# Optimization experiments

Hardware: AMD Instinct MI355X
Metric: run time of the kernel (lower is better)

The kernel has to match this reference:

```python
import jax, jax.numpy as jnp
import numpy as np
from jax import lax

SCORE_THRESHOLD = 0.001
IOU_THRESHOLD = 0.7
MAX_DETECTIONS = 300
PRE_NMS_TOPK = 1024      # standard pre-NMS candidate cap (torchvision/YOLO practice)
CLASS_OFFSET = 4096.0    # > max image coord, separates classes so cross-class IoU == 0
IMG = 640.0

B, N, C = 32, 8400, 80


def setup_inputs() -> dict:
    key = jax.random.key(0)
    kc, ks, kp = jax.random.split(key, 3)
    # well-formed boxes in [y1, x1, y2, x2] convention (matches repo's nms())
    tl = jax.random.uniform(kc, (B, N, 2), jnp.float32, 0.0, IMG - 1.0)   # (y1, x1)
    wh = jax.random.uniform(ks, (B, N, 2), jnp.float32, 4.0, 160.0)      # (h, w)
    boxes = jnp.concatenate([tl, jnp.minimum(tl + wh, IMG)], axis=-1)     # [B,N,4]
    scores = jax.random.uniform(kp, (B, N, C), jnp.float32)               # [B,N,C]
    return {"boxes": boxes, "scores": scores}


def _pairwise_iou(b):
    # b: [B,K,4] as [y1,x1,y2,x2]; +1 pixel convention per the repo's nms()
    y1, x1, y2, x2 = b[..., 0], b[..., 1], b[..., 2], b[..., 3]
    areas = (x2 - x1 + 1.0) * (y2 - y1 + 1.0)                             # [B,K]
    yy1 = jnp.maximum(y1[:, :, None], y1[:, None, :])
    xx1 = jnp.maximum(x1[:, :, None], x1[:, None, :])
    yy2 = jnp.minimum(y2[:, :, None], y2[:, None, :])
    xx2 = jnp.minimum(x2[:, :, None], x2[:, None, :])
    w = jnp.maximum(0.0, xx2 - xx1 + 1.0)
    h = jnp.maximum(0.0, yy2 - yy1 + 1.0)
    inter = w * h                                                          # [B,K,K]
    return inter / (areas[:, :, None] + areas[:, None, :] - inter)


def multiclass_nms(boxes, scores):
    b, n, c = scores.shape
    flat = jnp.where(scores > SCORE_THRESHOLD, scores, 0.0).reshape(b, n * c)
    top_scores, top_idx = lax.top_k(flat, PRE_NMS_TOPK)                    # [B,K]
    box_idx = top_idx // c
    cls_idx = top_idx % c                                                  # int32 [B,K]
    cand = jnp.take_along_axis(boxes, box_idx[..., None], axis=1)          # [B,K,4]
    # offset boxes by class so per-class NMS happens in one shared pass
    off = cand + (cls_idx.astype(cand.dtype) * CLASS_OFFSET)[..., None]
    iou = _pairwise_iou(off)                                               # [B,K,K]

    k = PRE_NMS_TOPK
    idx = jnp.arange(k)
    keep0 = top_scores > SCORE_THRESHOLD                                   # [B,K]

    def body(i, keep):
        row = iou[:, i, :]                                                 # [B,K]
        sup = (row > IOU_THRESHOLD) & keep[:, i][:, None] & (idx[None, :] > i)
        return keep & ~sup

    keep = lax.fori_loop(0, k, body, keep0)                                # greedy NMS

    final_scores = jnp.where(keep, top_scores, 0.0)
    out_scores, sel = lax.top_k(final_scores, MAX_DETECTIONS)              # [B,300]
    out_boxes = jnp.take_along_axis(cand, sel[..., None], axis=1)          # [B,300,4]
    out_labels = jnp.take_along_axis(cls_idx, sel, axis=1)                 # [B,300]
    n_valid = jnp.minimum(jnp.sum(keep, axis=1, keepdims=True), MAX_DETECTIONS)
    return out_boxes, out_scores, out_labels.astype(jnp.int32), n_valid.astype(jnp.int32)


def reference(boxes, scores):
    return multiclass_nms(boxes, scores)
```

## Files before the change

kernel.cpp:

```cpp
#include <hip/hip_runtime.h>
#include <cstdint>
#include <cstddef>

#define B_      32
#define N_      8400
#define C_      80
#define NC      672000
#define NCV4    168000
#define NBINS   4096
#define TOPK    1024
#define MAXDET  300
#define CANDCAP 4096
#define NSLICE  16
#define SLICE_V4 10500
#define STAGE_CAP 1024
#define CC_STRIDE 32

#define STAGE_THRESH 0.998046875f

#define WS_CANDCNT   0
#define WS_CANDKEYS  4096
#define WS_TOPSCORE  1052672
#define WS_TOPBOX    1183744
#define WS_TOPCLS    1708032
#define WS_KEEP      1839104
#define WS_TOTAL     1970176

#define OUT_SCORES  38400
#define OUT_LABELS  48000
#define OUT_NVALID  57600

__global__ __launch_bounds__(256) void stage_kernel(const float4* __restrict__ scores4,
                                                    unsigned* __restrict__ candCount,
                                                    unsigned long long* __restrict__ candKeys) {
    __shared__ unsigned long long stage[STAGE_CAP];
    __shared__ unsigned lcnt;
    __shared__ unsigned sbase;
    int b = blockIdx.x;
    int sl = blockIdx.y;
    int tid = threadIdx.x;
    if (tid == 0) lcnt = 0;
    __syncthreads();
    const float4* s = scores4 + (size_t)b * NCV4 + (size_t)sl * SLICE_V4;
    unsigned long long* ck = candKeys + (size_t)b * CANDCAP;
    unsigned* cc = &candCount[b * CC_STRIDE];
    for (int i = tid; i < SLICE_V4; i += 256) {
        float4 v = s[i];
        float c[4] = {v.x, v.y, v.z, v.w};
        unsigned flat0 = ((unsigned)sl * SLICE_V4 + (unsigned)i) * 4u;
        #pragma unroll
        for (int kc = 0; kc < 4; ++kc) {
            float x = (c[kc] > 0.001f) ? c[kc] : 0.0f;
            if (x >= STAGE_THRESH) {
                unsigned long long key =
                    ((unsigned long long)__float_as_uint(x) << 32) |
                    (unsigned long long)(0xFFFFFFFFu - (flat0 + kc));
                unsigned p = atomicAdd(&lcnt, 1u);
                if (p < (unsigned)STAGE_CAP) stage[p] = key;
                else {
                    unsigned gp = atomicAdd(cc, 1u);
                    if (gp < (unsigned)CANDCAP) ck[gp] = key;
                }
            }
        }
    }
    __syncthreads();
    unsigned n = lcnt < (unsigned)STAGE_CAP ? lcnt : (unsigned)STAGE_CAP;
    if (tid == 0) sbase = atomicAdd(cc, n);
    __syncthreads();
    unsigned basep = sbase;
    for (unsigned i = tid; i < n; i += 256) {
        unsigned gp = basep + i;
        if (gp < (unsigned)CANDCAP) ck[gp] = stage[i];
    }
}

__global__ __launch_bounds__(1024) void sort_gather_kernel(
        const float4* __restrict__ scores4,
        const unsigned long long* __restrict__ candKeys,
        const unsigned* __restrict__ candCount,
        const float* __restrict__ boxes,
        float* __restrict__ topScore,
        float* __restrict__ topBox,
        int* __restrict__ topCls) {
    __shared__ unsigned long long k[CANDCAP];
    __shared__ unsigned fhist[NBINS];
    __shared__ unsigned scnt;
    __shared__ int s_cut;
    int b = blockIdx.x;
    int tid = threadIdx.x;
    unsigned M = candCount[b * CC_STRIDE];
    bool fb = (M < (unsigned)TOPK) || (M > (unsigned)CANDCAP);
    int S;
    if (!fb) {
        S = (M <= 1024u) ? 1024 : (M <= 2048u ? 2048 : CANDCAP);
        const unsigned long long* ck = candKeys + (size_t)b * CANDCAP;
        for (int i = tid; i < S; i += 1024)
            k[i] = (i < (int)M) ? ck[i] : 0ull;
        __syncthreads();
    } else {
        for (int i = tid; i < NBINS; i += 1024) fhist[i] = 0;
        if (tid == 0) scnt = 0;
        __syncthreads();
        const float4* s = scores4 + (size_t)b * NCV4;
        for (int i = tid; i < NCV4; i += 1024) {
            float4 v = s[i];
            float c[4] = {v.x, v.y, v.z, v.w};
            #pragma unroll
            for (int kc = 0; kc < 4; ++kc) {
                float x = (c[kc] > 0.001f) ? c[kc] : 0.0f;
                int bin = (int)(x * 4096.0f);
                bin = bin > (NBINS - 1) ? (NBINS - 1) : bin;
                atomicAdd(&fhist[bin], 1u);
            }
        }
        __syncthreads();
        if (tid == 0) {
            unsigned acc = 0;
            int cb = 0;
            for (int bin = NBINS - 1; bin >= 0; --bin) {
                acc += fhist[bin];
                if (acc >= (unsigned)TOPK) { cb = bin; break; }
            }
            s_cut = cb;
        }
        __syncthreads();
        int cb = s_cut;
        for (int i = tid; i < NCV4; i += 1024) {
            float4 v = s[i];
            float c[4] = {v.x, v.y, v.z, v.w};
            unsigned flat0 = (unsigned)i * 4u;
            #pragma unroll
            for (int kc = 0; kc < 4; ++kc) {
                float x = (c[kc] > 0.001f) ? c[kc] : 0.0f;
                int bin = (int)(x * 4096.0f);
                bin = bin > (NBINS - 1) ? (NBINS - 1) : bin;
                if (bin >= cb) {
                    unsigned p = atomicAdd(&scnt, 1u);
                    if (p < (unsigned)CANDCAP)
                        k[p] = ((unsigned long long)__float_as_uint(x) << 32) |
                               (unsigned long long)(0xFFFFFFFFu - (flat0 + kc));
                }
            }
        }
        __syncthreads();
        unsigned M2 = scnt < (unsigned)CANDCAP ? scnt : (unsigned)CANDCAP;
        S = (M2 <= 1024u) ? 1024 : (M2 <= 2048u ? 2048 : CANDCAP);
        for (int i = tid; i < S; i += 1024)
            if (i >= (int)M2) k[i] = 0ull;
        __syncthreads();
    }
    for (int kk = 2; kk <= S; kk <<= 1) {
        for (int j = kk >> 1; j > 0; j >>= 1) {
            for (int t = tid; t < S; t += 1024) {
                int l = t ^ j;
                if (l > t) {
                    unsigned long long a = k[t], c = k[l];
                    bool sw = ((t & kk) == 0) ? (a < c) : (a > c);
                    if (sw) { k[t] = c; k[l] = a; }
                }
            }
            __syncthreads();
        }
    }
    int i = tid;
    unsigned long long key = k[i];
    float sc = __uint_as_float((unsigned)(key >> 32));
    unsigned idx = 0xFFFFFFFFu - (unsigned)(key & 0xFFFFFFFFull);
    if (idx >= (unsigned)NC) idx = 0;
    unsigned bi = idx / (unsigned)C_;
    unsigned cl = idx % (unsigned)C_;
    const float* bp = boxes + (size_t)b * N_ * 4 + (size_t)bi * 4;
    float c0 = bp[0], c1 = bp[1], c2 = bp[2], c3 = bp[3];
    topScore[b * TOPK + i] = sc;
    float* tb = topBox + ((size_t)b * TOPK + i) * 4;
    tb[0] = c0; tb[1] = c1; tb[2] = c2; tb[3] = c3;
    topCls[b * TOPK + i] = (int)cl;
}

#define CLS_CAP 256
__global__ __launch_bounds__(64) void nms_kernel(const float* __restrict__ topScore,
                                                 const float* __restrict__ topBox,
                                                 const int* __restrict__ topCls,
                                                 int* __restrict__ keep) {
    __shared__ unsigned short pos[CLS_CAP];
    __shared__ float by1[CLS_CAP], bx1[CLS_CAP], by2[CLS_CAP], bx2[CLS_CAP];
    __shared__ float barea[CLS_CAP];
    __shared__ unsigned char sup[CLS_CAP];
    int b = blockIdx.x;
    int c = blockIdx.y;
    int lane = threadIdx.x;
    const float* ts = topScore + b * TOPK;
    const int*   tc = topCls + b * TOPK;
    int*         kp = keep + b * TOPK;
    float off = (float)c * 4096.0f;
    int base = 0;
    for (int chunkS = 0; chunkS < TOPK; chunkS += 64) {
        int i = chunkS + lane;
        int cls = tc[i];
        float sc = ts[i];
        bool mine = (cls == c);
        bool listed = mine && (sc > 0.001f);
        if (mine) kp[i] = 0;
        unsigned long long mask = __ballot(listed);
        int rank = __popcll(mask & ((1ull << lane) - 1ull));
        if (listed) {
            int slot = base + rank;
            if (slot < CLS_CAP) {
                pos[slot] = (unsigned short)i;
                const float* tb = topBox + ((size_t)(b * TOPK + i)) * 4;
                float y1 = tb[0] + off, x1 = tb[1] + off;
                float y2 = tb[2] + off, x2 = tb[3] + off;
                by1[slot] = y1; bx1[slot] = x1; by2[slot] = y2; bx2[slot] = x2;
                barea[slot] = __fmul_rn((x2 - x1) + 1.0f, (y2 - y1) + 1.0f);
                sup[slot] = 0;
            }
        }
        base += __popcll(mask);
    }
    int m = base < CLS_CAP ? base : CLS_CAP;
    __syncthreads();
    int cur = 0;
    while (cur < m) {
        if (lane == 0) kp[pos[cur]] = 1;
        float cy1 = by1[cur], cx1 = bx1[cur], cy2 = by2[cur], cx2 = bx2[cur];
        float carea = barea[cur];
        for (int j = cur + 1 + lane; j < m; j += 64) {
            if (!sup[j]) {
                float yy1 = fmaxf(cy1, by1[j]), xx1 = fmaxf(cx1, bx1[j]);
                float yy2 = fminf(cy2, by2[j]), xx2 = fminf(cx2, bx2[j]);
                float w = fmaxf(0.0f, (xx2 - xx1) + 1.0f);
                float h = fmaxf(0.0f, (yy2 - yy1) + 1.0f);
                float inter = __fmul_rn(w, h);
                float denom = (carea + barea[j]) - inter;
                float iou = inter / denom;
                if (iou > 0.7f) sup[j] = 1;
            }
        }
        __syncthreads();
        int nxt = m;
        for (int j = cur + 1 + lane; j < m; j += 64)
            if (!sup[j]) { nxt = j; break; }
        for (int o = 32; o > 0; o >>= 1) {
            int other = __shfl_xor(nxt, o, 64);
            nxt = nxt < other ? nxt : other;
        }
        cur = nxt;
    }
}

__global__ __launch_bounds__(1024) void finalize_kernel(const float* __restrict__ topScore,
                                                        const float* __restrict__ topBox,
                                                        const int* __restrict__ topCls,
                                                        const int* __restrict__ keep,
                                                        float* __restrict__ out) {
    __shared__ int sk[TOPK];
    __shared__ int sel[MAXDET];
    int b = blockIdx.x;
    int i = threadIdx.x;
    int kp = keep[b * TOPK + i];
    sk[i] = kp;
    __syncthreads();
    for (int off = 1; off < TOPK; off <<= 1) {
        int add = (i >= off) ? sk[i - off] : 0;
        __syncthreads();
        sk[i] += add;
        __syncthreads();
    }
    int nk = sk[TOPK - 1];
    int incl = sk[i];
    int kexcl = incl - kp;
    int sexcl = i - kexcl;
    if (kp) {
        if (kexcl < MAXDET) sel[kexcl] = i;
    } else {
        int slot = nk + sexcl;
        if (slot < MAXDET) sel[slot] = i;
    }
    __syncthreads();
    if (i < MAXDET) {
        int p = sel[i];
        float sc = (i < nk) ? topScore[b * TOPK + p] : 0.0f;
        const float* tb = topBox + ((size_t)b * TOPK + p) * 4;
        float* ob = out + ((size_t)b * MAXDET + i) * 4;
        ob[0] = tb[0]; ob[1] = tb[1]; ob[2] = tb[2]; ob[3] = tb[3];
        out[OUT_SCORES + b * MAXDET + i] = sc;
        out[OUT_LABELS + b * MAXDET + i] = (float)topCls[b * TOPK + p];
    }
    if (i == 0) out[OUT_NVALID + b] = (float)(nk < MAXDET ? nk : MAXDET);
}

extern "C" void kernel_launch(void* const* d_in, const int* in_sizes, int n_in,
                              void* d_out, int out_size, void* d_ws, size_t ws_size,
                              hipStream_t stream) {
    const float* boxes  = (const float*)d_in[0];
    const float* scores = (const float*)d_in[1];
    float* out = (float*)d_out;
    char* ws = (char*)d_ws;

    unsigned* candCount = (unsigned*)(ws + WS_CANDCNT);
    unsigned long long* candKeys = (unsigned long long*)(ws + WS_CANDKEYS);
    float* topScore = (float*)(ws + WS_TOPSCORE);
    float* topBox = (float*)(ws + WS_TOPBOX);
    int* topCls = (int*)(ws + WS_TOPCLS);
    int* keep = (int*)(ws + WS_KEEP);

    const float4* scores4 = (const float4*)scores;

    hipMemsetAsync(candCount, 0, B_ * CC_STRIDE * sizeof(unsigned), stream);

    stage_kernel<<<dim3(B_, NSLICE), 256, 0, stream>>>(scores4, candCount, candKeys);
    sort_gather_kernel<<<B_, 1024, 0, stream>>>(scores4, candKeys, candCount, boxes,
                                                topScore, topBox, topCls);
    nms_kernel<<<dim3(B_, C_), 64, 0, stream>>>(topScore, topBox, topCls, keep);
    finalize_kernel<<<B_, 1024, 0, stream>>>(topScore, topBox, topCls, keep, out);
}
```

Baseline: 202.3 us.

## Fuse sort, NMS and finalize into one per-batch kernel with per-slice segments

```diff
diff --git a/kernel.cpp b/kernel.cpp
--- a/kernel.cpp
+++ b/kernel.cpp
@@ -13,37 +13,26 @@
 #define CANDCAP 4096
 #define NSLICE  16
 #define SLICE_V4 10500
-#define STAGE_CAP 1024
-#define CC_STRIDE 32
+#define SEGCAP  256
 
 #define STAGE_THRESH 0.998046875f
 
-#define WS_CANDCNT   0
-#define WS_CANDKEYS  4096
-#define WS_TOPSCORE  1052672
-#define WS_TOPBOX    1183744
-#define WS_TOPCLS    1708032
-#define WS_KEEP      1839104
-#define WS_TOTAL     1970176
+#define WS_CANDKEYS  0
+#define WS_SEGCNT    1048576
 
 #define OUT_SCORES  38400
 #define OUT_LABELS  48000
 #define OUT_NVALID  57600
 
 __global__ __launch_bounds__(256) void stage_kernel(const float4* __restrict__ scores4,
-                                                    unsigned* __restrict__ candCount,
+                                                    unsigned* __restrict__ segCnt,
                                                     unsigned long long* __restrict__ candKeys) {
-    __shared__ unsigned long long stage[STAGE_CAP];
     __shared__ unsigned lcnt;
-    __shared__ unsigned sbase;
-    int b = blockIdx.x;
-    int sl = blockIdx.y;
-    int tid = threadIdx.x;
+    int b = blockIdx.x, sl = blockIdx.y, tid = threadIdx.x;
     if (tid == 0) lcnt = 0;
     __syncthreads();
     const float4* s = scores4 + (size_t)b * NCV4 + (size_t)sl * SLICE_V4;
-    unsigned long long* ck = candKeys + (size_t)b * CANDCAP;
-    unsigned* cc = &candCount[b * CC_STRIDE];
+    unsigned long long* seg = candKeys + (size_t)b * CANDCAP + (size_t)sl * SEGCAP;
     for (int i = tid; i < SLICE_V4; i += 256) {
         float4 v = s[i];
         float c[4] = {v.x, v.y, v.z, v.w};
@@ -52,242 +41,257 @@
         for (int kc = 0; kc < 4; ++kc) {
             float x = (c[kc] > 0.001f) ? c[kc] : 0.0f;
             if (x >= STAGE_THRESH) {
-                unsigned long long key =
-                    ((unsigned long long)__float_as_uint(x) << 32) |
-                    (unsigned long long)(0xFFFFFFFFu - (flat0 + kc));
                 unsigned p = atomicAdd(&lcnt, 1u);
-                if (p < (unsigned)STAGE_CAP) stage[p] = key;
-                else {
-                    unsigned gp = atomicAdd(cc, 1u);
-                    if (gp < (unsigned)CANDCAP) ck[gp] = key;
-                }
-            }
-        }
-    }
-    __syncthreads();
-    unsigned n = lcnt < (unsigned)STAGE_CAP ? lcnt : (unsigned)STAGE_CAP;
-    if (tid == 0) sbase = atomicAdd(cc, n);
-    __syncthreads();
-    unsigned basep = sbase;
-    for (unsigned i = tid; i < n; i += 256) {
-        unsigned gp = basep + i;
-        if (gp < (unsigned)CANDCAP) ck[gp] = stage[i];
-    }
+                if (p < (unsigned)SEGCAP)
+                    seg[p] = ((unsigned long long)__float_as_uint(x) << 32) |
+                             (unsigned long long)(0xFFFFFFFFu - (flat0 + kc));
+            }
+        }
+    }
+    __syncthreads();
+    if (tid == 0) segCnt[b * NSLICE + sl] = lcnt;
 }
 
-__global__ __launch_bounds__(1024) void sort_gather_kernel(
+struct PhaseA {
+    unsigned long long k[CANDCAP];
+    unsigned fhist[NBINS];
+    unsigned scnt;
+    int cut;
+};
+struct PhaseB {
+    float sc[TOPK];
+    float oy1[TOPK], ox1[TOPK], oy2[TOPK], ox2[TOPK];
+    float area[TOPK];
+    float4 ob[TOPK];
+    unsigned short cls[TOPK];
+    int keep[TOPK];
+    unsigned short wps[16][TOPK];
+    int sel[MAXDET];
+};
+
+__global__ __launch_bounds__(1024) void mega_kernel(
         const float4* __restrict__ scores4,
         const unsigned long long* __restrict__ candKeys,
-        const unsigned* __restrict__ candCount,
-        const float* __restrict__ boxes,
-        float* __restrict__ topScore,
-        float* __restrict__ topBox,
-        int* __restrict__ topCls) {
-    __shared__ unsigned long long k[CANDCAP];
-    __shared__ unsigned fhist[NBINS];
-    __shared__ unsigned scnt;
-    __shared__ int s_cut;
+        const unsigned* __restrict__ segCnt,
+        const float4* __restrict__ boxes4,
+        float* __restrict__ out) {
+    __shared__ union { PhaseA a; PhaseB bb; } u;
+    __shared__ unsigned pref[NSLICE + 1];
+    __shared__ int s_fb;
     int b = blockIdx.x;
     int tid = threadIdx.x;
-    unsigned M = candCount[b * CC_STRIDE];
-    bool fb = (M < (unsigned)TOPK) || (M > (unsigned)CANDCAP);
-    int S;
-    if (!fb) {
-        S = (M <= 1024u) ? 1024 : (M <= 2048u ? 2048 : CANDCAP);
-        const unsigned long long* ck = candKeys + (size_t)b * CANDCAP;
-        for (int i = tid; i < S; i += 1024)
-            k[i] = (i < (int)M) ? ck[i] : 0ull;
-        __syncthreads();
+
+    if (tid < NSLICE) pref[tid + 1] = segCnt[b * NSLICE + tid];
+    __syncthreads();
+    if (tid == 0) {
+        unsigned acc = 0; int fb2 = 0;
+        pref[0] = 0;
+        for (int s2 = 1; s2 <= NSLICE; ++s2) {
+            unsigned c2 = pref[s2];
+            if (c2 > (unsigned)SEGCAP) fb2 = 1;
+            acc += c2;
+            pref[s2] = acc;
+        }
+        if (acc < (unsigned)TOPK || acc > (unsigned)CANDCAP) fb2 = 1;
+        s_fb = fb2;
+    }
+    __syncthreads();
+
+    unsigned M;
+    if (!s_fb) {
+        for (int s2 = 0; s2 < NSLICE; ++s2) {
+            unsigned base2 = pref[s2], n2 = pref[s2 + 1] - base2;
+            const unsigned long long* src =
+                candKeys + (size_t)b * CANDCAP + (size_t)s2 * SEGCAP;
+            for (unsigned t = tid; t < n2; t += 1024) u.a.k[base2 + t] = src[t];
+        }
+        M = pref[NSLICE];
     } else {
-        for (int i = tid; i < NBINS; i += 1024) fhist[i] = 0;
-        if (tid == 0) scnt = 0;
+        for (int i2 = tid; i2 < NBINS; i2 += 1024) u.a.fhist[i2] = 0;
+        if (tid == 0) u.a.scnt = 0;
         __syncthreads();
         const float4* s = scores4 + (size_t)b * NCV4;
-        for (int i = tid; i < NCV4; i += 1024) {
-            float4 v = s[i];
-            float c[4] = {v.x, v.y, v.z, v.w};
+        for (int i2 = tid; i2 < NCV4; i2 += 1024) {
+            float4 v = s[i2];
+            float c4[4] = {v.x, v.y, v.z, v.w};
             #pragma unroll
             for (int kc = 0; kc < 4; ++kc) {
-                float x = (c[kc] > 0.001f) ? c[kc] : 0.0f;
+                float x = (c4[kc] > 0.001f) ? c4[kc] : 0.0f;
                 int bin = (int)(x * 4096.0f);
                 bin = bin > (NBINS - 1) ? (NBINS - 1) : bin;
-                atomicAdd(&fhist[bin], 1u);
+                atomicAdd(&u.a.fhist[bin], 1u);
             }
         }
         __syncthreads();
         if (tid == 0) {
-            unsigned acc = 0;
-            int cb = 0;
+            unsigned acc = 0; int cb = 0;
             for (int bin = NBINS - 1; bin >= 0; --bin) {
-                acc += fhist[bin];
+                acc += u.a.fhist[bin];
                 if (acc >= (unsigned)TOPK) { cb = bin; break; }
             }
-            s_cut = cb;
-        }
-        __syncthreads();
-        int cb = s_cut;
-        for (int i = tid; i < NCV4; i += 1024) {
-            float4 v = s[i];
-            float c[4] = {v.x, v.y, v.z, v.w};
-            unsigned flat0 = (unsigned)i * 4u;
+            u.a.cut = cb;
+        }
+        __syncthreads();
+        int cb = u.a.cut;
+        for (int i2 = tid; i2 < NCV4; i2 += 1024) {
+            float4 v = s[i2];
+            float c4[4] = {v.x, v.y, v.z, v.w};
+            unsigned flat0 = (unsigned)i2 * 4u;
             #pragma unroll
             for (int kc = 0; kc < 4; ++kc) {
-                float x = (c[kc] > 0.001f) ? c[kc] : 0.0f;
+                float x = (c4[kc] > 0.001f) ? c4[kc] : 0.0f;
                 int bin = (int)(x * 4096.0f);
                 bin = bin > (NBINS - 1) ? (NBINS - 1) : bin;
                 if (bin >= cb) {
-                    unsigned p = atomicAdd(&scnt, 1u);
+                    unsigned p = atomicAdd(&u.a.scnt, 1u);
                     if (p < (unsigned)CANDCAP)
-                        k[p] = ((unsigned long long)__float_as_uint(x) << 32) |
-                               (unsigned long long)(0xFFFFFFFFu - (flat0 + kc));
-                }
-            }
-        }
-        __syncthreads();
-        unsigned M2 = scnt < (unsigned)CANDCAP ? scnt : (unsigned)CANDCAP;
-        S = (M2 <= 1024u) ? 1024 : (M2 <= 2048u ? 2048 : CANDCAP);
-        for (int i = tid; i < S; i += 1024)
-            if (i >= (int)M2) k[i] = 0ull;
-        __syncthreads();
-    }
-    for (int kk = 2; kk <= S; kk <<= 1) {
-        for (int j = kk >> 1; j > 0; j >>= 1) {
-            for (int t = tid; t < S; t += 1024) {
-                int l = t ^ j;
-                if (l > t) {
-                    unsigned long long a = k[t], c = k[l];
-                    bool sw = ((t & kk) == 0) ? (a < c) : (a > c);
-                    if (sw) { k[t] = c; k[l] = a; }
-                }
-            }
+                        u.a.k[p] = ((unsigned long long)__float_as_uint(x) << 32) |
+                                   (unsigned long long)(0xFFFFFFFFu - (flat0 + kc));
+                }
+            }
+        }
+        __syncthreads();
+        M = u.a.scnt;
+        if (M > (unsigned)CANDCAP) M = CANDCAP;
+    }
+    int S = (M <= 1024u) ? 1024 : (M <= 2048u ? 2048 : CANDCAP);
+    for (int i2 = tid; i2 < S; i2 += 1024)
+        if (i2 >= (int)M) u.a.k[i2] = 0ull;
+    __syncthreads();
+
+    {
+        bool crossed = false;
+        for (int kk = 2; kk <= S; kk <<= 1) {
+            int j = kk >> 1;
+            for (; j >= 128; j >>= 1) {
+                __syncthreads();
+                for (int t = tid; t < S; t += 1024) {
+                    int l = t ^ j;
+                    if (l > t) {
+                        unsigned long long a0 = u.a.k[t], c0 = u.a.k[l];
+                        bool sw = ((t & kk) == 0) ? (a0 < c0) : (a0 > c0);
+                        if (sw) { u.a.k[t] = c0; u.a.k[l] = a0; }
+                    }
+                }
+                crossed = true;
+            }
+            if (crossed) { __syncthreads(); crossed = false; }
+            int half = S >> 1;
+            for (; j >= 1; j >>= 1) {
+                for (int c2 = tid; c2 < half; c2 += 1024) {
+                    int t = ((c2 & ~(j - 1)) << 1) | (c2 & (j - 1));
+                    int l = t | j;
+                    unsigned long long a0 = u.a.k[t], c0 = u.a.k[l];
+                    bool sw = ((t & kk) == 0) ? (a0 < c0) : (a0 > c0);
+                    if (sw) { u.a.k[t] = c0; u.a.k[l] = a0; }
+                }
+                __threadfence_block();
+            }
+        }
+    }
+    __syncthreads();
+
+    unsigned long long key = u.a.k[tid];
+    __syncthreads();
+    {
+        float sc = __uint_as_float((unsigned)(key >> 32));
+        unsigned idx = 0xFFFFFFFFu - (unsigned)(key & 0xFFFFFFFFull);
+        if (idx >= (unsigned)NC) idx = 0;
+        unsigned bi = idx / (unsigned)C_;
+        unsigned cl = idx - bi * (unsigned)C_;
+        float4 bx = boxes4[(size_t)b * N_ + bi];
+        float off = (float)cl * 4096.0f;
+        float oy1 = bx.x + off, ox1 = bx.y + off;
+        float oy2 = bx.z + off, ox2 = bx.w + off;
+        u.bb.sc[tid] = sc;
+        u.bb.oy1[tid] = oy1; u.bb.ox1[tid] = ox1;
+        u.bb.oy2[tid] = oy2; u.bb.ox2[tid] = ox2;
+        u.bb.area[tid] = __fmul_rn((ox2 - ox1) + 1.0f, (oy2 - oy1) + 1.0f);
+        u.bb.ob[tid] = bx;
+        u.bb.cls[tid] = (unsigned short)cl;
+        u.bb.keep[tid] = 0;
+    }
+    __syncthreads();
+
+    {
+        int w = tid >> 6, lane = tid & 63;
+        unsigned long long lmask = (1ull << lane) - 1ull;
+        unsigned short* wp = u.bb.wps[w];
+        for (int cc = w * 5; cc < w * 5 + 5; ++cc) {
+            int nm = 0;
+            for (int chunk = 0; chunk < TOPK; chunk += 64) {
+                int i2 = chunk + lane;
+                bool listed = (u.bb.cls[i2] == (unsigned short)cc) &&
+                              (u.bb.sc[i2] > 0.001f);
+                unsigned long long mask = __ballot(listed);
+                if (listed) wp[nm + __popcll(mask & lmask)] = (unsigned short)i2;
+                nm += __popcll(mask);
+            }
+            __threadfence_block();
+            int cur = 0;
+            while (cur < nm) {
+                int pcur = wp[cur] & 0x3FF;
+                if (lane == 0) u.bb.keep[pcur] = 1;
+                float cy1 = u.bb.oy1[pcur], cx1 = u.bb.ox1[pcur];
+                float cy2 = u.bb.oy2[pcur], cx2 = u.bb.ox2[pcur];
+                float carea = u.bb.area[pcur];
+                for (int t2 = cur + 1 + lane; t2 < nm; t2 += 64) {
+                    unsigned short e = wp[t2];
+                    if (!(e & 0x8000)) {
+                        int pj = e;
+                        float yy1 = fmaxf(cy1, u.bb.oy1[pj]);
+                        float xx1 = fmaxf(cx1, u.bb.ox1[pj]);
+                        float yy2 = fminf(cy2, u.bb.oy2[pj]);
+                        float xx2 = fminf(cx2, u.bb.ox2[pj]);
+                        float w2 = fmaxf(0.0f, (xx2 - xx1) + 1.0f);
+                        float h2 = fmaxf(0.0f, (yy2 - yy1) + 1.0f);
+                        float inter = __fmul_rn(w2, h2);
+                        float denom = (carea + u.bb.area[pj]) - inter;
+                        if (inter / denom > 0.7f) wp[t2] = e | 0x8000;
+                    }
+                }
+                __threadfence_block();
+                int nxt = nm;
+                for (int t2 = cur + 1 + lane; t2 < nm; t2 += 64)
+                    if (!(wp[t2] & 0x8000)) { nxt = t2; break; }
+                for (int o = 32; o > 0; o >>= 1) {
+                    int other = __shfl_xor(nxt, o, 64);
+                    nxt = nxt < other ? nxt : other;
+                }
+                cur = nxt;
+            }
+        }
+    }
+    __syncthreads();
+
+    {
+        int kp = u.bb.keep[tid];
+        for (int off2 = 1; off2 < TOPK; off2 <<= 1) {
+            int add = (tid >= off2) ? u.bb.keep[tid - off2] : 0;
             __syncthreads();
-        }
-    }
-    int i = tid;
-    unsigned long long key = k[i];
-    float sc = __uint_as_float((unsigned)(key >> 32));
-    unsigned idx = 0xFFFFFFFFu - (unsigned)(key & 0xFFFFFFFFull);
-    if (idx >= (unsigned)NC) idx = 0;
-    unsigned bi = idx / (unsigned)C_;
-    unsigned cl = idx % (unsigned)C_;
-    const float* bp = boxes + (size_t)b * N_ * 4 + (size_t)bi * 4;
-    float c0 = bp[0], c1 = bp[1], c2 = bp[2], c3 = bp[3];
-    topScore[b * TOPK + i] = sc;
-    float* tb = topBox + ((size_t)b * TOPK + i) * 4;
-    tb[0] = c0; tb[1] = c1; tb[2] = c2; tb[3] = c3;
-    topCls[b * TOPK + i] = (int)cl;
-}
-
-#define CLS_CAP 256
-__global__ __launch_bounds__(64) void nms_kernel(const float* __restrict__ topScore,
-                                                 const float* __restrict__ topBox,
-                                                 const int* __restrict__ topCls,
-                                                 int* __restrict__ keep) {
-    __shared__ unsigned short pos[CLS_CAP];
-    __shared__ float by1[CLS_CAP], bx1[CLS_CAP], by2[CLS_CAP], bx2[CLS_CAP];
-    __shared__ float barea[CLS_CAP];
-    __shared__ unsigned char sup[CLS_CAP];
-    int b = blockIdx.x;
-    int c = blockIdx.y;
-    int lane = threadIdx.x;
-    const float* ts = topScore + b * TOPK;
-    const int*   tc = topCls + b * TOPK;
-    int*         kp = keep + b * TOPK;
-    float off = (float)c * 4096.0f;
-    int base = 0;
-    for (int chunkS = 0; chunkS < TOPK; chunkS += 64) {
-        int i = chunkS + lane;
-        int cls = tc[i];
-        float sc = ts[i];
-        bool mine = (cls == c);
-        bool listed = mine && (sc > 0.001f);
-        if (mine) kp[i] = 0;
-        unsigned long long mask = __ballot(listed);
-        int rank = __popcll(mask & ((1ull << lane) - 1ull));
-        if (listed) {
-            int slot = base + rank;
-            if (slot < CLS_CAP) {
-                pos[slot] = (unsigned short)i;
-                const float* tb = topBox + ((size_t)(b * TOPK + i)) * 4;
-                float y1 = tb[0] + off, x1 = tb[1] + off;
-                float y2 = tb[2] + off, x2 = tb[3] + off;
-                by1[slot] = y1; bx1[slot] = x1; by2[slot] = y2; bx2[slot] = x2;
-                barea[slot] = __fmul_rn((x2 - x1) + 1.0f, (y2 - y1) + 1.0f);
-                sup[slot] = 0;
-            }
-        }
-        base += __popcll(mask);
-    }
-    int m = base < CLS_CAP ? base : CLS_CAP;
-    __syncthreads();
-    int cur = 0;
-    while (cur < m) {
-        if (lane == 0) kp[pos[cur]] = 1;
-        float cy1 = by1[cur], cx1 = bx1[cur], cy2 = by2[cur], cx2 = bx2[cur];
-        float carea = barea[cur];
-        for (int j = cur + 1 + lane; j < m; j += 64) {
-            if (!sup[j]) {
-                float yy1 = fmaxf(cy1, by1[j]), xx1 = fmaxf(cx1, bx1[j]);
-                float yy2 = fminf(cy2, by2[j]), xx2 = fminf(cx2, bx2[j]);
-                float w = fmaxf(0.0f, (xx2 - xx1) + 1.0f);
-                float h = fmaxf(0.0f, (yy2 - yy1) + 1.0f);
-                float inter = __fmul_rn(w, h);
-                float denom = (carea + barea[j]) - inter;
-                float iou = inter / denom;
-                if (iou > 0.7f) sup[j] = 1;
-            }
-        }
-        __syncthreads();
-        int nxt = m;
-        for (int j = cur + 1 + lane; j < m; j += 64)
-            if (!sup[j]) { nxt = j; break; }
-        for (int o = 32; o > 0; o >>= 1) {
-            int other = __shfl_xor(nxt, o, 64);
-            nxt = nxt < other ? nxt : other;
-        }
-        cur = nxt;
-    }
-}
-
-__global__ __launch_bounds__(1024) void finalize_kernel(const float* __restrict__ topScore,
-                                                        const float* __restrict__ topBox,
-                                                        const int* __restrict__ topCls,
-                                                        const int* __restrict__ keep,
-                                                        float* __restrict__ out) {
-    __shared__ int sk[TOPK];
-    __shared__ int sel[MAXDET];
-    int b = blockIdx.x;
-    int i = threadIdx.x;
-    int kp = keep[b * TOPK + i];
-    sk[i] = kp;
-    __syncthreads();
-    for (int off = 1; off < TOPK; off <<= 1) {
-        int add = (i >= off) ? sk[i - off] : 0;
-        __syncthreads();
-        sk[i] += add;
-        __syncthreads();
-    }
-    int nk = sk[TOPK - 1];
-    int incl = sk[i];
-    int kexcl = incl - kp;
-    int sexcl = i - kexcl;
-    if (kp) {
-        if (kexcl < MAXDET) sel[kexcl] = i;
-    } else {
-        int slot = nk + sexcl;
-        if (slot < MAXDET) sel[slot] = i;
-    }
-    __syncthreads();
-    if (i < MAXDET) {
-        int p = sel[i];
-        float sc = (i < nk) ? topScore[b * TOPK + p] : 0.0f;
-        const float* tb = topBox + ((size_t)b * TOPK + p) * 4;
-        float* ob = out + ((size_t)b * MAXDET + i) * 4;
-        ob[0] = tb[0]; ob[1] = tb[1]; ob[2] = tb[2]; ob[3] = tb[3];
-        out[OUT_SCORES + b * MAXDET + i] = sc;
-        out[OUT_LABELS + b * MAXDET + i] = (float)topCls[b * TOPK + p];
-    }
-    if (i == 0) out[OUT_NVALID + b] = (float)(nk < MAXDET ? nk : MAXDET);
+            u.bb.keep[tid] += add;
+            __syncthreads();
+        }
+        int nk = u.bb.keep[TOPK - 1];
+        int incl = u.bb.keep[tid];
+        int kexcl = incl - kp;
+        int sexcl = tid - kexcl;
+        if (kp) {
+            if (kexcl < MAXDET) u.bb.sel[kexcl] = tid;
+        } else {
+            int slot = nk + sexcl;
+            if (slot < MAXDET) u.bb.sel[slot] = tid;
+        }
+        __syncthreads();
+        if (tid < MAXDET) {
+            int p = u.bb.sel[tid];
+            float sc2 = (tid < nk) ? u.bb.sc[p] : 0.0f;
+            ((float4*)out)[b * MAXDET + tid] = u.bb.ob[p];
+            out[OUT_SCORES + b * MAXDET + tid] = sc2;
+            out[OUT_LABELS + b * MAXDET + tid] = (float)u.bb.cls[p];
+        }
+        if (tid == 0) out[OUT_NVALID + b] = (float)(nk < MAXDET ? nk : MAXDET);
+    }
 }
 
 extern "C" void kernel_launch(void* const* d_in, const int* in_sizes, int n_in,
@@ -298,20 +302,12 @@
     float* out = (float*)d_out;
     char* ws = (char*)d_ws;
 
-    unsigned* candCount = (unsigned*)(ws + WS_CANDCNT);
     unsigned long long* candKeys = (unsigned long long*)(ws + WS_CANDKEYS);
-    float* topScore = (float*)(ws + WS_TOPSCORE);
-    float* topBox = (float*)(ws + WS_TOPBOX);
-    int* topCls = (int*)(ws + WS_TOPCLS);
-    int* keep = (int*)(ws + WS_KEEP);
+    unsigned* segCnt = (unsigned*)(ws + WS_SEGCNT);
 
     const float4* scores4 = (const float4*)scores;
-
-    hipMemsetAsync(candCount, 0, B_ * CC_STRIDE * sizeof(unsigned), stream);
-
-    stage_kernel<<<dim3(B_, NSLICE), 256, 0, stream>>>(scores4, candCount, candKeys);
-    sort_gather_kernel<<<B_, 1024, 0, stream>>>(scores4, candKeys, candCount, boxes,
-                                                topScore, topBox, topCls);
-    nms_kernel<<<dim3(B_, C_), 64, 0, stream>>>(topScore, topBox, topCls, keep);
-    finalize_kernel<<<B_, 1024, 0, stream>>>(topScore, topBox, topCls, keep, out);
+    const float4* boxes4  = (const float4*)boxes;
+
+    stage_kernel<<<dim3(B_, NSLICE), 256, 0, stream>>>(scores4, segCnt, candKeys);
+    mega_kernel<<<B_, 1024, 0, stream>>>(scores4, candKeys, segCnt, boxes4, out);
 }
```

Result: slower. 223.2 us (+10.3%).

## Use per-slice candidate segments, drop memset, and elide intra-wave sort barriers

Applied to the files above, without the earlier changes.

```diff
diff --git a/kernel.cpp b/kernel.cpp
--- a/kernel.cpp
+++ b/kernel.cpp
@@ -13,37 +13,30 @@
 #define CANDCAP 4096
 #define NSLICE  16
 #define SLICE_V4 10500
-#define STAGE_CAP 1024
-#define CC_STRIDE 32
+#define SEGCAP  256
 
 #define STAGE_THRESH 0.998046875f
 
-#define WS_CANDCNT   0
-#define WS_CANDKEYS  4096
-#define WS_TOPSCORE  1052672
-#define WS_TOPBOX    1183744
-#define WS_TOPCLS    1708032
-#define WS_KEEP      1839104
-#define WS_TOTAL     1970176
+#define WS_CANDKEYS  0
+#define WS_SEGCNT    1048576
+#define WS_TOPSCORE  1050624
+#define WS_TOPBOX    1181696
+#define WS_TOPCLS    1705984
+#define WS_KEEP      1837056
 
 #define OUT_SCORES  38400
 #define OUT_LABELS  48000
 #define OUT_NVALID  57600
 
 __global__ __launch_bounds__(256) void stage_kernel(const float4* __restrict__ scores4,
-                                                    unsigned* __restrict__ candCount,
+                                                    unsigned* __restrict__ segCnt,
                                                     unsigned long long* __restrict__ candKeys) {
-    __shared__ unsigned long long stage[STAGE_CAP];
     __shared__ unsigned lcnt;
-    __shared__ unsigned sbase;
-    int b = blockIdx.x;
-    int sl = blockIdx.y;
-    int tid = threadIdx.x;
+    int b = blockIdx.x, sl = blockIdx.y, tid = threadIdx.x;
     if (tid == 0) lcnt = 0;
     __syncthreads();
     const float4* s = scores4 + (size_t)b * NCV4 + (size_t)sl * SLICE_V4;
-    unsigned long long* ck = candKeys + (size_t)b * CANDCAP;
-    unsigned* cc = &candCount[b * CC_STRIDE];
+    unsigned long long* seg = candKeys + (size_t)b * CANDCAP + (size_t)sl * SEGCAP;
     for (int i = tid; i < SLICE_V4; i += 256) {
         float4 v = s[i];
         float c[4] = {v.x, v.y, v.z, v.w};
@@ -52,124 +45,136 @@
         for (int kc = 0; kc < 4; ++kc) {
             float x = (c[kc] > 0.001f) ? c[kc] : 0.0f;
             if (x >= STAGE_THRESH) {
-                unsigned long long key =
-                    ((unsigned long long)__float_as_uint(x) << 32) |
-                    (unsigned long long)(0xFFFFFFFFu - (flat0 + kc));
                 unsigned p = atomicAdd(&lcnt, 1u);
-                if (p < (unsigned)STAGE_CAP) stage[p] = key;
-                else {
-                    unsigned gp = atomicAdd(cc, 1u);
-                    if (gp < (unsigned)CANDCAP) ck[gp] = key;
-                }
-            }
-        }
-    }
-    __syncthreads();
-    unsigned n = lcnt < (unsigned)STAGE_CAP ? lcnt : (unsigned)STAGE_CAP;
-    if (tid == 0) sbase = atomicAdd(cc, n);
-    __syncthreads();
-    unsigned basep = sbase;
-    for (unsigned i = tid; i < n; i += 256) {
-        unsigned gp = basep + i;
-        if (gp < (unsigned)CANDCAP) ck[gp] = stage[i];
-    }
+                if (p < (unsigned)SEGCAP)
+                    seg[p] = ((unsigned long long)__float_as_uint(x) << 32) |
+                             (unsigned long long)(0xFFFFFFFFu - (flat0 + kc));
+            }
+        }
+    }
+    __syncthreads();
+    if (tid == 0) segCnt[b * NSLICE + sl] = lcnt;
 }
 
 __global__ __launch_bounds__(1024) void sort_gather_kernel(
         const float4* __restrict__ scores4,
         const unsigned long long* __restrict__ candKeys,
-        const unsigned* __restrict__ candCount,
+        const unsigned* __restrict__ segCnt,
         const float* __restrict__ boxes,
         float* __restrict__ topScore,
         float* __restrict__ topBox,
         int* __restrict__ topCls) {
-    __shared__ unsigned long long k[CANDCAP];
-    __shared__ unsigned fhist[NBINS];
+    __shared__ union {
+        unsigned long long k[CANDCAP];
+        unsigned fh[2 * CANDCAP];
+    } u;
+    __shared__ unsigned pref[NSLICE + 1];
+    __shared__ int s_fb;
     __shared__ unsigned scnt;
     __shared__ int s_cut;
     int b = blockIdx.x;
     int tid = threadIdx.x;
-    unsigned M = candCount[b * CC_STRIDE];
-    bool fb = (M < (unsigned)TOPK) || (M > (unsigned)CANDCAP);
-    int S;
-    if (!fb) {
-        S = (M <= 1024u) ? 1024 : (M <= 2048u ? 2048 : CANDCAP);
-        const unsigned long long* ck = candKeys + (size_t)b * CANDCAP;
-        for (int i = tid; i < S; i += 1024)
-            k[i] = (i < (int)M) ? ck[i] : 0ull;
-        __syncthreads();
+
+    if (tid < NSLICE) pref[tid + 1] = segCnt[b * NSLICE + tid];
+    __syncthreads();
+    if (tid == 0) {
+        unsigned acc = 0; int fb2 = 0;
+        pref[0] = 0;
+        for (int s2 = 1; s2 <= NSLICE; ++s2) {
+            unsigned c2 = pref[s2];
+            if (c2 > (unsigned)SEGCAP) fb2 = 1;
+            acc += c2;
+            pref[s2] = acc;
+        }
+        if (acc < (unsigned)TOPK || acc > (unsigned)CANDCAP) fb2 = 1;
+        s_fb = fb2;
+    }
+    __syncthreads();
+
+    unsigned M;
+    if (!s_fb) {
+        int w = tid >> 6, lane = tid & 63;
+        unsigned base2 = pref[w], n2 = pref[w + 1] - base2;
+        const unsigned long long* src =
+            candKeys + (size_t)b * CANDCAP + (size_t)w * SEGCAP;
+        for (unsigned t = lane; t < n2; t += 64) u.k[base2 + t] = src[t];
+        M = pref[NSLICE];
     } else {
-        for (int i = tid; i < NBINS; i += 1024) fhist[i] = 0;
+        for (int i2 = tid; i2 < NBINS; i2 += 1024) u.fh[i2] = 0;
         if (tid == 0) scnt = 0;
         __syncthreads();
         const float4* s = scores4 + (size_t)b * NCV4;
-        for (int i = tid; i < NCV4; i += 1024) {
-            float4 v = s[i];
-            float c[4] = {v.x, v.y, v.z, v.w};
+        for (int i2 = tid; i2 < NCV4; i2 += 1024) {
+            float4 v = s[i2];
+            float c4[4] = {v.x, v.y, v.z, v.w};
             #pragma unroll
             for (int kc = 0; kc < 4; ++kc) {
-                float x = (c[kc] > 0.001f) ? c[kc] : 0.0f;
+                float x = (c4[kc] > 0.001f) ? c4[kc] : 0.0f;
                 int bin = (int)(x * 4096.0f);
                 bin = bin > (NBINS - 1) ? (NBINS - 1) : bin;
-                atomicAdd(&fhist[bin], 1u);
+                atomicAdd(&u.fh[bin], 1u);
             }
         }
         __syncthreads();
         if (tid == 0) {
-            unsigned acc = 0;
-            int cb = 0;
+            unsigned acc = 0; int cb = 0;
             for (int bin = NBINS - 1; bin >= 0; --bin) {
-                acc += fhist[bin];
+                acc += u.fh[bin];
                 if (acc >= (unsigned)TOPK) { cb = bin; break; }
             }
             s_cut = cb;
         }
         __syncthreads();
         int cb = s_cut;
-        for (int i = tid; i < NCV4; i += 1024) {
-            float4 v = s[i];
-            float c[4] = {v.x, v.y, v.z, v.w};
-            unsigned flat0 = (unsigned)i * 4u;
+        for (int i2 = tid; i2 < NCV4; i2 += 1024) {
+            float4 v = s[i2];
+            float c4[4] = {v.x, v.y, v.z, v.w};
+            unsigned flat0 = (unsigned)i2 * 4u;
             #pragma unroll
             for (int kc = 0; kc < 4; ++kc) {
-                float x = (c[kc] > 0.001f) ? c[kc] : 0.0f;
+                float x = (c4[kc] > 0.001f) ? c4[kc] : 0.0f;
                 int bin = (int)(x * 4096.0f);
                 bin = bin > (NBINS - 1) ? (NBINS - 1) : bin;
                 if (bin >= cb) {
                     unsigned p = atomicAdd(&scnt, 1u);
                     if (p < (unsigned)CANDCAP)
-                        k[p] = ((unsigned long long)__float_as_uint(x) << 32) |
-                               (unsigned long long)(0xFFFFFFFFu - (flat0 + kc));
+                        u.k[p] = ((unsigned long long)__float_as_uint(x) << 32) |
+                                 (unsigned long long)(0xFFFFFFFFu - (flat0 + kc));
                 }
             }
         }
         __syncthreads();
-        unsigned M2 = scnt < (unsigned)CANDCAP ? scnt : (unsigned)CANDCAP;
-        S = (M2 <= 1024u) ? 1024 : (M2 <= 2048u ? 2048 : CANDCAP);
-        for (int i = tid; i < S; i += 1024)
-            if (i >= (int)M2) k[i] = 0ull;
-        __syncthreads();
-    }
+        M = scnt;
+        if (M > (unsigned)CANDCAP) M = CANDCAP;
+    }
+    int S = (M <= 1024u) ? 1024 : (M <= 2048u ? 2048 : CANDCAP);
+    for (int i2 = tid; i2 < S; i2 += 1024)
+        if (i2 >= (int)M) u.k[i2] = 0ull;
+    __syncthreads();
+
     for (int kk = 2; kk <= S; kk <<= 1) {
         for (int j = kk >> 1; j > 0; j >>= 1) {
+            if (j >= 32) __syncthreads();
+            else         __threadfence_block();
             for (int t = tid; t < S; t += 1024) {
                 int l = t ^ j;
                 if (l > t) {
-                    unsigned long long a = k[t], c = k[l];
-                    bool sw = ((t & kk) == 0) ? (a < c) : (a > c);
-                    if (sw) { k[t] = c; k[l] = a; }
+                    unsigned long long a0 = u.k[t], c0 = u.k[l];
+                    bool sw = ((t & kk) == 0) ? (a0 < c0) : (a0 > c0);
+                    if (sw) { u.k[t] = c0; u.k[l] = a0; }
                 }
             }
-            __syncthreads();
-        }
-    }
+        }
+    }
+    __syncthreads();
+
     int i = tid;
-    unsigned long long key = k[i];
+    unsigned long long key = u.k[i];
     float sc = __uint_as_float((unsigned)(key >> 32));
     unsigned idx = 0xFFFFFFFFu - (unsigned)(key & 0xFFFFFFFFull);
     if (idx >= (unsigned)NC) idx = 0;
     unsigned bi = idx / (unsigned)C_;
-    unsigned cl = idx % (unsigned)C_;
+    unsigned cl = idx - bi * (unsigned)C_;
     const float* bp = boxes + (size_t)b * N_ * 4 + (size_t)bi * 4;
     float c0 = bp[0], c1 = bp[1], c2 = bp[2], c3 = bp[3];
     topScore[b * TOPK + i] = sc;
@@ -298,8 +303,8 @@
     float* out = (float*)d_out;
     char* ws = (char*)d_ws;
 
-    unsigned* candCount = (unsigned*)(ws + WS_CANDCNT);
     unsigned long long* candKeys = (unsigned long long*)(ws + WS_CANDKEYS);
+    unsigned* segCnt = (unsigned*)(ws + WS_SEGCNT);
     float* topScore = (float*)(ws + WS_TOPSCORE);
     float* topBox = (float*)(ws + WS_TOPBOX);
     int* topCls = (int*)(ws + WS_TOPCLS);
@@ -307,10 +312,8 @@
 
     const float4* scores4 = (const float4*)scores;
 
-    hipMemsetAsync(candCount, 0, B_ * CC_STRIDE * sizeof(unsigned), stream);
-
-    stage_kernel<<<dim3(B_, NSLICE), 256, 0, stream>>>(scores4, candCount, candKeys);
-    sort_gather_kernel<<<B_, 1024, 0, stream>>>(scores4, candKeys, candCount, boxes,
+    stage_kernel<<<dim3(B_, NSLICE), 256, 0, stream>>>(scores4, segCnt, candKeys);
+    sort_gather_kernel<<<B_, 1024, 0, stream>>>(scores4, candKeys, segCnt, boxes,
                                                 topScore, topBox, topCls);
     nms_kernel<<<dim3(B_, C_), 64, 0, stream>>>(topScore, topBox, topCls, keep);
     finalize_kernel<<<B_, 1024, 0, stream>>>(topScore, topBox, topCls, keep, out);
```

Measured after the change: 198.6 us. No clear change (-1.9%).
